# Kernel tuning notes

Hardware: AMD Instinct MI355X
Metric: run time of the kernel (lower is better)

## Reference

```python
import jax, jax.numpy as jnp
import numpy as np

B, S, E, H = 4, 2048, 1024, 16
HD = E // H


def setup_inputs() -> dict:
    key = jax.random.key(0)
    ks = jax.random.split(key, 7)
    scale = 1.0 / np.sqrt(E)
    return {
        "query": jax.random.normal(ks[0], (B, S, E), dtype=jnp.float32),
        "key": jax.random.normal(ks[1], (B, S, E), dtype=jnp.float32),
        "value": jax.random.normal(ks[2], (B, S, E), dtype=jnp.float32),
        "Wqkv": jax.random.normal(ks[3], (3 * E, E), dtype=jnp.float32) * scale,
        "bqkv": jnp.zeros((3 * E,), dtype=jnp.float32),
        "Wout": jax.random.normal(ks[4], (E, E), dtype=jnp.float32) * scale,
        "bout": jnp.zeros((E,), dtype=jnp.float32),
    }


def reference(query, key, value, Wqkv, bqkv, Wout, bout):
    # key/value are ignored by the original module (QKV all from query).
    b, s, e = query.shape
    qkv = query @ Wqkv.T + bqkv                       # [B,S,3E]
    qkv = qkv.reshape(b, s, 3, H, HD)
    q = jnp.transpose(qkv[:, :, 0], (0, 2, 1, 3))     # [B,H,S,HD]
    k = jnp.transpose(qkv[:, :, 1], (0, 2, 1, 3))
    v = jnp.transpose(qkv[:, :, 2], (0, 2, 1, 3))
    # NOTE: original scales by embed_dim**0.5, not head_dim**0.5
    scores = jnp.einsum("bhqd,bhkd->bhqk", q, k) / jnp.sqrt(jnp.float32(e))
    attn = jax.nn.softmax(scores, axis=-1)            # dropout = identity (eval)
    out = jnp.einsum("bhqk,bhkd->bhqd", attn, v)      # [B,H,S,HD]
    out = jnp.transpose(out, (0, 2, 1, 3)).reshape(b, s, e)
    return out @ Wout.T + bout
```

## Files before the change

kernel.cpp:

```cpp
#include <hip/hip_runtime.h>
#include <stdint.h>


typedef __bf16 bf16;
typedef __bf16 bf16x8 __attribute__((ext_vector_type(8)));
typedef __bf16 bf16x4 __attribute__((ext_vector_type(4)));
typedef float  f32x4  __attribute__((ext_vector_type(4)));
typedef float  f32x16 __attribute__((ext_vector_type(16)));
typedef unsigned u32x2 __attribute__((ext_vector_type(2)));
typedef unsigned u32x4 __attribute__((ext_vector_type(4)));

#define MFMA16(a, b, c) __builtin_amdgcn_mfma_f32_16x16x32_bf16((a), (b), (c), 0, 0, 0)
#define MFMA32(a, b, c) __builtin_amdgcn_mfma_f32_32x32x16_bf16((a), (b), (c), 0, 0, 0)

__device__ __forceinline__ void gload16(const void* g, void* l) {
  __builtin_amdgcn_global_load_lds(
      (const __attribute__((address_space(1))) void*)g,
      (__attribute__((address_space(3))) void*)l, 16, 0, 0);
}

__device__ __forceinline__ uint32_t lds_off(const void* p) {
  return (uint32_t)(uintptr_t)(__attribute__((address_space(3))) const void*)p;
}

__device__ __forceinline__ bf16x4 tr16(uint32_t off) {
  bf16x4 d;
  asm volatile("ds_read_b64_tr_b16 %0, %1" : "=&v"(d) : "v"(off));
  return d;
}
template <int IMM>
__device__ __forceinline__ bf16x4 tr16o(uint32_t off) {
  bf16x4 d;
  asm volatile("ds_read_b64_tr_b16 %0, %1 offset:%2" : "=&v"(d) : "v"(off), "i"(IMM));
  return d;
}

__device__ __forceinline__ bf16x8 vpack(bf16x4 lo, bf16x4 hi) {
  const u32x2 a = __builtin_bit_cast(u32x2, lo);
  const u32x2 b = __builtin_bit_cast(u32x2, hi);
  u32x4 t;
  t[0] = a[0]; t[1] = a[1]; t[2] = b[0]; t[3] = b[1];
  return __builtin_bit_cast(bf16x8, t);
}

__global__ __launch_bounds__(256) void cvt_all(const float* __restrict__ a,
                                               const float* __restrict__ b,
                                               const float* __restrict__ c,
                                               bf16* __restrict__ out,
                                               int na4, int nb4, int nc4) {
  const int i = blockIdx.x * 256 + threadIdx.x;
  const float4* src;
  int j = i;
  if (i < na4) {
    src = (const float4*)a;
  } else if (i < na4 + nb4) {
    src = (const float4*)b; j = i - na4;
  } else if (i < na4 + nb4 + nc4) {
    src = (const float4*)c; j = i - na4 - nb4;
  } else {
    return;
  }
  const float4 v = src[j];
  bf16x4 o;
  o[0] = (bf16)v.x; o[1] = (bf16)v.y; o[2] = (bf16)v.z; o[3] = (bf16)v.w;
  ((bf16x4*)out)[i] = o;
}

template <typename OutT>
__global__ __launch_bounds__(256, 2) void gemm_bt(const bf16* __restrict__ A,
                                                  const bf16* __restrict__ Bt,
                                                  const float* __restrict__ bias,
                                                  OutT* __restrict__ C,
                                                  int M, int N, int K,
                                                  int sc_lo, int sc_hi, float scv) {
  __shared__ bf16 As[128 * 32];
  __shared__ bf16 Bs[128 * 32];
  const int tid = threadIdx.x;
  const int lane = tid & 63, wid = tid >> 6;
  const int l15 = lane & 15, lg = lane >> 4;
  const int wr = wid >> 1, wc = wid & 1;
  const int row0 = blockIdx.y * 128, col0 = blockIdx.x * 128;
  const float cscale = (col0 >= sc_lo && col0 < sc_hi) ? scv : 1.0f;

  f32x4 acc[4][4];
#pragma unroll
  for (int m = 0; m < 4; ++m)
#pragma unroll
    for (int n = 0; n < 4; ++n) acc[m][n] = (f32x4){0.f, 0.f, 0.f, 0.f};

  for (int k0 = 0; k0 < K; k0 += 32) {
    __syncthreads();
#pragma unroll
    for (int j = 0; j < 2; ++j) {
      const int c = j * 256 + tid;
      const int r = c >> 2, cb = (c & 3) << 4;
      gload16((const char*)(A + (size_t)(row0 + r) * K + k0) + cb, (char*)As + c * 16);
      gload16((const char*)(Bt + (size_t)(col0 + r) * K + k0) + cb, (char*)Bs + c * 16);
    }
    __syncthreads();

    bf16x8 af[4], bfr[4];
#pragma unroll
    for (int m = 0; m < 4; ++m)
      af[m] = *(const bf16x8*)(As + ((wr * 64 + m * 16 + l15) << 5) + lg * 8);
#pragma unroll
    for (int n = 0; n < 4; ++n)
      bfr[n] = *(const bf16x8*)(Bs + ((wc * 64 + n * 16 + l15) << 5) + lg * 8);
#pragma unroll
    for (int m = 0; m < 4; ++m)
#pragma unroll
      for (int n = 0; n < 4; ++n) acc[m][n] = MFMA16(af[m], bfr[n], acc[m][n]);
  }

#pragma unroll
  for (int m = 0; m < 4; ++m) {
    const int grow0 = row0 + wr * 64 + m * 16 + lg * 4;
#pragma unroll
    for (int n = 0; n < 4; ++n) {
      const int gcol = col0 + wc * 64 + n * 16 + l15;
      const float bv = bias[gcol];
#pragma unroll
      for (int i = 0; i < 4; ++i)
        C[(size_t)(grow0 + i) * N + gcol] = (OutT)((acc[m][n][i] + bv) * cscale);
    }
  }
}

__global__ __launch_bounds__(512, 4) void attn_fwd(const bf16* __restrict__ qkv,
                                                   bf16* __restrict__ aout) {
  __shared__ bf16 Ks[2][64 * 64];
  __shared__ bf16 Vs[2][64 * 64];
  __shared__ float bc[8][32];

  const int bid = blockIdx.x;
  const int xcd = bid & 7, slot = bid >> 3;
  const int g = xcd + 8 * (slot >> 3);
  const int qblk = slot & 7;
  const int h = g & 15, b = g >> 4;

  const int tid = threadIdx.x, wid = tid >> 6, lane = tid & 63;
  const int l31 = lane & 31, hh = lane >> 5, l15 = lane & 15;
  const int b4 = (lane >> 4) & 1;
  const bf16* qbase = qkv + (size_t)b * 2048 * 3072;

  bf16x8 qf[4];
  {
    const bf16* qp = qbase + (size_t)(qblk * 256 + wid * 32 + l31) * 3072 + h * 64 + hh * 8;
    qf[0] = *(const bf16x8*)(qp);
    qf[1] = *(const bf16x8*)(qp + 16);
    qf[2] = *(const bf16x8*)(qp + 32);
    qf[3] = *(const bf16x8*)(qp + 48);
  }

  const char* ksrc; const char* vsrc;
  int kdo, vdo;
  {
    const int c = tid;
    {
      const int key = c >> 3;
      const int db = (((c & 7) ^ (key & 7)) << 4);
      ksrc = (const char*)(qbase + (size_t)key * 3072 + 1024 + h * 64) + db;
      kdo = c * 16;
    }
    {
      const int s = c >> 3, jj = c & 7;
      const int vkey = ((s >> 2) << 2) + (jj >> 1);
      const int vd = ((s & 3) << 4) + ((jj & 1) << 3);
      vsrc = (const char*)(qbase + (size_t)vkey * 3072 + 2048 + h * 64 + vd);
      vdo = c * 16;
    }
  }
  const size_t tadv = (size_t)64 * 3072 * 2;

  f32x16 o0, o1;
#pragma unroll
  for (int i = 0; i < 16; ++i) { o0[i] = 0.f; o1[i] = 0.f; }
  float lrow = 0.f;

  const uint32_t vbase = lds_off(&Vs[0][0]) + (uint32_t)(l15 * 8 + hh * 1024 + b4 * 128);

  gload16(ksrc, (char*)&Ks[0][0] + kdo);
  gload16(vsrc, (char*)&Vs[0][0] + vdo);

  for (int kt = 0; kt < 32; ++kt) {
    const int cur = kt & 1;
    if (kt < 31) {
      const size_t off = (size_t)(kt + 1) * tadv;
      gload16(ksrc + off, (char*)&Ks[cur ^ 1][0] + kdo);
      gload16(vsrc + off, (char*)&Vs[cur ^ 1][0] + vdo);
      __builtin_amdgcn_sched_barrier(0);
      asm volatile("s_waitcnt vmcnt(2)" ::: "memory");
    } else {
      __builtin_amdgcn_sched_barrier(0);
      asm volatile("s_waitcnt vmcnt(0)" ::: "memory");
    }
    __builtin_amdgcn_s_barrier();
    __builtin_amdgcn_sched_barrier(0);

    const char* ksb = (const char*)&Ks[cur][0];
    const uint32_t vb_cur = vbase + (uint32_t)(cur * 8192);

    f32x16 st0, st1;
#pragma unroll
    for (int i = 0; i < 16; ++i) { st0[i] = 0.f; st1[i] = 0.f; }
    __builtin_amdgcn_s_setprio(1);
#pragma unroll
    for (int k2 = 0; k2 < 4; ++k2) {
      const int dby = k2 * 32 + hh * 16;
      bf16x8 kf0 = *(const bf16x8*)(ksb + ((l31 * 128 + dby) ^ ((l31 & 7) << 4)));
      st0 = MFMA32(kf0, qf[k2], st0);
      bf16x8 kf1 = *(const bf16x8*)(ksb + (((l31 + 32) * 128 + dby) ^ ((l31 & 7) << 4)));
      st1 = MFMA32(kf1, qf[k2], st1);
    }
    __builtin_amdgcn_s_setprio(0);

    float ps0 = 0.f, ps1 = 0.f;
#pragma unroll
    for (int i = 0; i < 16; ++i) {
      st0[i] = __builtin_amdgcn_exp2f(st0[i]);
      st1[i] = __builtin_amdgcn_exp2f(st1[i]);
      ps0 += st0[i];
      ps1 += st1[i];
    }
    float ps = ps0 + ps1;
    ps += __shfl_xor(ps, 32);
    lrow += ps;

    uint32_t w[16];
#pragma unroll
    for (int j = 0; j < 8; ++j) {
      asm("v_cvt_pk_bf16_f32 %0, %1, %2" : "=v"(w[j]) : "v"(st0[2 * j]), "v"(st0[2 * j + 1]));
      asm("v_cvt_pk_bf16_f32 %0, %1, %2" : "=v"(w[8 + j]) : "v"(st1[2 * j]), "v"(st1[2 * j + 1]));
    }
#pragma unroll
    for (int g2 = 0; g2 < 4; ++g2) {
      asm volatile("v_permlane32_swap_b32 %0, %1" : "+v"(w[4 * g2]), "+v"(w[4 * g2 + 2]));
      asm volatile("v_permlane32_swap_b32 %0, %1" : "+v"(w[4 * g2 + 1]), "+v"(w[4 * g2 + 3]));
    }
    bf16x8 pf[4];
#pragma unroll
    for (int k2 = 0; k2 < 4; ++k2) {
      u32x4 t;
      t[0] = w[4 * k2]; t[1] = w[4 * k2 + 1]; t[2] = w[4 * k2 + 2]; t[3] = w[4 * k2 + 3];
      pf[k2] = __builtin_bit_cast(bf16x8, t);
    }

    {
      bf16x4 va[4], vb2[4];
      va[0] = tr16o<0 * 2048 + 0>(vb_cur);
      vb2[0] = tr16o<0 * 2048 + 512>(vb_cur);
      va[1] = tr16o<1 * 2048 + 0>(vb_cur);
      vb2[1] = tr16o<1 * 2048 + 512>(vb_cur);
      va[2] = tr16o<2 * 2048 + 0>(vb_cur);
      vb2[2] = tr16o<2 * 2048 + 512>(vb_cur);
      va[3] = tr16o<3 * 2048 + 0>(vb_cur);
      vb2[3] = tr16o<3 * 2048 + 512>(vb_cur);
      asm volatile("s_waitcnt lgkmcnt(0)" ::: "memory");
      __builtin_amdgcn_sched_barrier(0);
      __builtin_amdgcn_s_setprio(1);
#pragma unroll
      for (int k2 = 0; k2 < 4; ++k2)
        o0 = MFMA32(pf[k2], vpack(va[k2], vb2[k2]), o0);
      __builtin_amdgcn_s_setprio(0);
      va[0] = tr16o<0 * 2048 + 256 + 0>(vb_cur);
      vb2[0] = tr16o<0 * 2048 + 256 + 512>(vb_cur);
      va[1] = tr16o<1 * 2048 + 256 + 0>(vb_cur);
      vb2[1] = tr16o<1 * 2048 + 256 + 512>(vb_cur);
      va[2] = tr16o<2 * 2048 + 256 + 0>(vb_cur);
      vb2[2] = tr16o<2 * 2048 + 256 + 512>(vb_cur);
      va[3] = tr16o<3 * 2048 + 256 + 0>(vb_cur);
      vb2[3] = tr16o<3 * 2048 + 256 + 512>(vb_cur);
      asm volatile("s_waitcnt lgkmcnt(0)" ::: "memory");
      __builtin_amdgcn_sched_barrier(0);
      __builtin_amdgcn_s_setprio(1);
#pragma unroll
      for (int k2 = 0; k2 < 4; ++k2)
        o1 = MFMA32(pf[k2], vpack(va[k2], vb2[k2]), o1);
      __builtin_amdgcn_s_setprio(0);
    }
    __builtin_amdgcn_sched_barrier(0);
    __builtin_amdgcn_s_barrier();
  }

  if (lane < 32) bc[wid][l31] = 1.0f / lrow;
  bf16* ob = aout + ((size_t)b * 2048 + qblk * 256 + wid * 32) * 1024 + h * 64;
#pragma unroll
  for (int r = 0; r < 16; ++r) {
    const int row = (r & 3) + 8 * (r >> 2) + 4 * hh;
    const float inv = bc[wid][row];
    ob[(size_t)row * 1024 + l31]      = (bf16)(o0[r] * inv);
    ob[(size_t)row * 1024 + 32 + l31] = (bf16)(o1[r] * inv);
  }
}

extern "C" void kernel_launch(void* const* d_in, const int* in_sizes, int n_in,
                              void* d_out, int out_size, void* d_ws, size_t ws_size,
                              hipStream_t stream) {
  const float* query = (const float*)d_in[0];
  const float* Wqkv = (const float*)d_in[3];
  const float* bqkv = (const float*)d_in[4];
  const float* Wout = (const float*)d_in[5];
  const float* bout = (const float*)d_in[6];
  float* out = (float*)d_out;

  constexpr int M = 8192;
  constexpr int E = 1024, E3 = 3072;
  constexpr float SC = 0.045084220f;

  bf16* q_bf    = (bf16*)d_ws;
  bf16* wqkv_bf = q_bf + (size_t)M * E;
  bf16* wout_bf = wqkv_bf + (size_t)E3 * E;
  bf16* qkv_bf  = wout_bf + (size_t)E * E;
  bf16* aout_bf = qkv_bf + (size_t)M * E3;

  constexpr int na4 = M * E / 4, nb4 = E3 * E / 4, nc4 = E * E / 4;
  cvt_all<<<(na4 + nb4 + nc4 + 255) / 256, 256, 0, stream>>>(
      query, Wqkv, Wout, q_bf, na4, nb4, nc4);

  gemm_bt<bf16><<<dim3(E3 / 128, M / 128), 256, 0, stream>>>(
      q_bf, wqkv_bf, bqkv, qkv_bf, M, E3, E, E, 2 * E, SC);
  attn_fwd<<<512, 512, 0, stream>>>(qkv_bf, aout_bf);
  gemm_bt<float><<<dim3(E / 128, M / 128), 256, 0, stream>>>(
      aout_bf, wout_bf, bout, out, M, E, E, 0, 0, 1.0f);
}
```

Before: 196.8 us.

## Double-buffer GEMM LDS tiles with async prefetch and explicit waitcnt

```diff
diff --git a/kernel.cpp b/kernel.cpp
--- a/kernel.cpp
+++ b/kernel.cpp
@@ -23,11 +23,6 @@
   return (uint32_t)(uintptr_t)(__attribute__((address_space(3))) const void*)p;
 }
 
-__device__ __forceinline__ bf16x4 tr16(uint32_t off) {
-  bf16x4 d;
-  asm volatile("ds_read_b64_tr_b16 %0, %1" : "=&v"(d) : "v"(off));
-  return d;
-}
 template <int IMM>
 __device__ __forceinline__ bf16x4 tr16o(uint32_t off) {
   bf16x4 d;
@@ -73,8 +68,8 @@
                                                   OutT* __restrict__ C,
                                                   int M, int N, int K,
                                                   int sc_lo, int sc_hi, float scv) {
-  __shared__ bf16 As[128 * 32];
-  __shared__ bf16 Bs[128 * 32];
+  __shared__ bf16 As[2][128 * 32];
+  __shared__ bf16 Bs[2][128 * 32];
   const int tid = threadIdx.x;
   const int lane = tid & 63, wid = tid >> 6;
   const int l15 = lane & 15, lg = lane >> 4;
@@ -82,34 +77,64 @@
   const int row0 = blockIdx.y * 128, col0 = blockIdx.x * 128;
   const float cscale = (col0 >= sc_lo && col0 < sc_hi) ? scv : 1.0f;
 
+  const char* asrc[2]; const char* bsrc[2];
+  int ado[2];
+#pragma unroll
+  for (int j = 0; j < 2; ++j) {
+    const int c = j * 256 + tid;
+    const int r = c >> 2, cb = (c & 3) << 4;
+    asrc[j] = (const char*)(A + (size_t)(row0 + r) * K) + cb;
+    bsrc[j] = (const char*)(Bt + (size_t)(col0 + r) * K) + cb;
+    ado[j] = c * 16;
+  }
+
   f32x4 acc[4][4];
 #pragma unroll
   for (int m = 0; m < 4; ++m)
 #pragma unroll
     for (int n = 0; n < 4; ++n) acc[m][n] = (f32x4){0.f, 0.f, 0.f, 0.f};
 
-  for (int k0 = 0; k0 < K; k0 += 32) {
-    __syncthreads();
-#pragma unroll
-    for (int j = 0; j < 2; ++j) {
-      const int c = j * 256 + tid;
-      const int r = c >> 2, cb = (c & 3) << 4;
-      gload16((const char*)(A + (size_t)(row0 + r) * K + k0) + cb, (char*)As + c * 16);
-      gload16((const char*)(Bt + (size_t)(col0 + r) * K + k0) + cb, (char*)Bs + c * 16);
-    }
-    __syncthreads();
-
+  const int nIt = K >> 5;
+
+  gload16(asrc[0], (char*)&As[0][0] + ado[0]);
+  gload16(asrc[1], (char*)&As[0][0] + ado[1]);
+  gload16(bsrc[0], (char*)&Bs[0][0] + ado[0]);
+  gload16(bsrc[1], (char*)&Bs[0][0] + ado[1]);
+
+  for (int it = 0; it < nIt; ++it) {
+    const int cur = it & 1;
+    if (it < nIt - 1) {
+      const size_t off = (size_t)(it + 1) * 64;
+      gload16(asrc[0] + off, (char*)&As[cur ^ 1][0] + ado[0]);
+      gload16(asrc[1] + off, (char*)&As[cur ^ 1][0] + ado[1]);
+      gload16(bsrc[0] + off, (char*)&Bs[cur ^ 1][0] + ado[0]);
+      gload16(bsrc[1] + off, (char*)&Bs[cur ^ 1][0] + ado[1]);
+      __builtin_amdgcn_sched_barrier(0);
+      asm volatile("s_waitcnt vmcnt(4)" ::: "memory");
+    } else {
+      __builtin_amdgcn_sched_barrier(0);
+      asm volatile("s_waitcnt vmcnt(0)" ::: "memory");
+    }
+    __builtin_amdgcn_s_barrier();
+    __builtin_amdgcn_sched_barrier(0);
+
+    const bf16* as = &As[cur][0];
+    const bf16* bs = &Bs[cur][0];
     bf16x8 af[4], bfr[4];
 #pragma unroll
     for (int m = 0; m < 4; ++m)
-      af[m] = *(const bf16x8*)(As + ((wr * 64 + m * 16 + l15) << 5) + lg * 8);
+      af[m] = *(const bf16x8*)(as + ((wr * 64 + m * 16 + l15) << 5) + lg * 8);
 #pragma unroll
     for (int n = 0; n < 4; ++n)
-      bfr[n] = *(const bf16x8*)(Bs + ((wc * 64 + n * 16 + l15) << 5) + lg * 8);
+      bfr[n] = *(const bf16x8*)(bs + ((wc * 64 + n * 16 + l15) << 5) + lg * 8);
+    __builtin_amdgcn_s_setprio(1);
 #pragma unroll
     for (int m = 0; m < 4; ++m)
 #pragma unroll
       for (int n = 0; n < 4; ++n) acc[m][n] = MFMA16(af[m], bfr[n], acc[m][n]);
+    __builtin_amdgcn_s_setprio(0);
+    __builtin_amdgcn_sched_barrier(0);
+    __builtin_amdgcn_s_barrier();
   }
 
 #pragma unroll
```

New measurement: 189.8 us. 3.6% less time.
